# Performance work log

Hardware: AMD Instinct MI355X
Metric: run time of the kernel (lower is better)

The kernel has to match this reference:

```python
import jax, jax.numpy as jnp
import numpy as np

ATTN_SCALE = 0.12  # attn_args.attn_scale (constant hyperparameter)
EPS = 1e-6         # F.rms_norm eps
GATE_IN = 12       # attn_gate input features (x[..., :12])


def rms_norm(x):
    return x * jax.lax.rsqrt(jnp.mean(x * x, axis=-1, keepdims=True) + EPS)


def rotary(x, cos, sin):
    # x: [B,T,H,D]; cos/sin: [T,D//2]
    x1, x2 = jnp.split(x, 2, axis=-1)
    c = cos[None, :, None, :]
    s = sin[None, :, None, :]
    return jnp.concatenate([x1 * c + x2 * s, -x1 * s + x2 * c], axis=-1)


def setup_inputs() -> dict:
    key = jax.random.key(0)
    ks = jax.random.split(key, 5)
    B, T, D, H, HD = 1, 2048, 1024, 8, 128
    std = 0.5 * D ** -0.5
    x = jax.random.normal(ks[0], (B, T, D), jnp.float32)
    qkvo_w = jax.random.normal(ks[1], (4, D, D), jnp.float32) * std
    gate_w = jax.random.normal(ks[2], (H, GATE_IN), jnp.float32) * 0.02
    ve = jax.random.normal(ks[3], (B, T, H, HD), jnp.float32)
    sa_lambdas = jax.random.uniform(ks[4], (2,), jnp.float32, 0.3, 0.7)
    half = HD // 2
    inv_freq = 1.0 / (10000.0 ** (jnp.arange(half, dtype=jnp.float32) / half))
    ang = jnp.arange(T, dtype=jnp.float32)[:, None] * inv_freq[None, :]
    return dict(x=x, qkvo_w=qkvo_w, gate_w=gate_w, ve=ve,
                sa_lambdas=sa_lambdas, cos=jnp.cos(ang), sin=jnp.sin(ang))


def reference(x, qkvo_w, gate_w, ve, sa_lambdas, cos, sin):
    B, T, D = x.shape
    H = gate_w.shape[0]
    HD = D // H
    # fused QKV projection: rows of qkvo_w[:3] are [q; k; v]
    w_qkv = qkvo_w[:3].reshape(3 * D, D)           # [3D, D]
    qkv = jnp.einsum('btd,ed->bte', x, w_qkv)      # [B,T,3D]
    qkv = qkv.reshape(B, T, 3, H, HD)
    q, k, v = qkv[:, :, 0], qkv[:, :, 1], qkv[:, :, 2]
    # RMSNorm + RoPE on q, k
    q = rotary(rms_norm(q), cos, sin)
    k = rotary(rms_norm(k), cos, sin)
    # value-residual mixing
    v = sa_lambdas[0] * v + sa_lambdas[1] * ve
    # causal SDPA with custom scale
    scores = jnp.einsum('bqhd,bkhd->bhqk', q, k) * ATTN_SCALE
    causal = jnp.tril(jnp.ones((T, T), dtype=bool))
    scores = jnp.where(causal[None, None], scores, jnp.finfo(scores.dtype).min)
    p = jax.nn.softmax(scores, axis=-1)
    y = jnp.einsum('bhqk,bkhd->bqhd', p, v)        # [B,T,H,HD]
    # per-head sigmoid gate from the first 12 channels of x
    gate = jax.nn.sigmoid(jnp.einsum('bti,hi->bth', x[..., :GATE_IN], gate_w))
    y = y * gate[..., None]
    # output projection (qkvo_w[3]): F.linear -> y @ W_o^T
    out = jnp.einsum('bti,oi->bto', y.reshape(B, T, H * HD), qkvo_w[3])
    return out
```

## Files before the change

### kernel.cpp

```cpp
#include <hip/hip_runtime.h>
#include <stdint.h>

typedef unsigned short u16;
typedef unsigned int u32;

typedef __bf16 bfx8 __attribute__((ext_vector_type(8)));
typedef float fx4 __attribute__((ext_vector_type(4)));
typedef float fx16 __attribute__((ext_vector_type(16)));
typedef u16 u16x4 __attribute__((ext_vector_type(4)));
typedef u16 u16x8 __attribute__((ext_vector_type(8)));

#define GAS __attribute__((address_space(1)))
#define LAS __attribute__((address_space(3)))

__device__ __forceinline__ void gload16(const void* g, void* l) {
  __builtin_amdgcn_global_load_lds((GAS void*)g, (LAS void*)l, 16, 0, 0);
}

__device__ __forceinline__ u16 f2bf(float f) {
  union { float f; u32 u; } v; v.f = f;
  u32 r = v.u + 0x7fffu + ((v.u >> 16) & 1u);
  return (u16)(r >> 16);
}
__device__ __forceinline__ float bf2f(u16 u) {
  union { u32 u; float f; } v; v.u = ((u32)u) << 16;
  return v.f;
}

__device__ __forceinline__ int segF(int qb) { return (qb * qb + 2 * qb + (qb & 1)) >> 2; }

__global__ __launch_bounds__(256) void k_cvt(const float* __restrict__ src, u16* __restrict__ dst, int n) {
  int i = (blockIdx.x * 256 + threadIdx.x) * 8;
  if (i >= n) return;
  const float4* s = (const float4*)(src + i);
  float4 a = s[0], b = s[1];
  u16x8 o;
  o[0] = f2bf(a.x); o[1] = f2bf(a.y); o[2] = f2bf(a.z); o[3] = f2bf(a.w);
  o[4] = f2bf(b.x); o[5] = f2bf(b.y); o[6] = f2bf(b.z); o[7] = f2bf(b.w);
  *(u16x8*)(dst + i) = o;
}

__global__ __launch_bounds__(256) void k_gemm_out(const u16* __restrict__ A, const u16* __restrict__ B,
                                                  float* __restrict__ C, int M, int N, int K) {
  __shared__ char sm[16384];
  const int tid = threadIdx.x;
  const int l = tid & 63, w = tid >> 6;
  const int li = l & 15, lg = l >> 4;
  const int bid = (blockIdx.x & 7) * 64 + (blockIdx.x >> 3);
  const int nbm = M >> 6;
  const int bm = bid % nbm, bn = bid / nbm;

  const u16* gsrc[4];
#pragma unroll
  for (int i = 0; i < 4; ++i) {
    int b = i * 4096 + tid * 16;
    int row, ch;
    const u16* mat;
    if (b < 8192) { row = b >> 7; mat = A + (size_t)(bm * 64 + row) * K; }
    else          { int bb = b - 8192; row = bb >> 7; mat = B + (size_t)(bn * 64 + row) * K; }
    ch = ((b >> 4) & 7) ^ (row & 7);
    gsrc[i] = mat + ch * 8;
  }

  fx4 acc[4];
#pragma unroll
  for (int jj = 0; jj < 4; ++jj)
#pragma unroll
    for (int r = 0; r < 4; ++r) acc[jj][r] = 0.f;

  for (int k0 = 0; k0 < K; k0 += 64) {
    __syncthreads();
#pragma unroll
    for (int i = 0; i < 4; ++i) gload16(gsrc[i] + k0, sm + i * 4096 + w * 1024);
    __syncthreads();
#pragma unroll
    for (int kk = 0; kk < 2; ++kk) {
      int rowa = w * 16 + li;
      bfx8 af = *(const bfx8*)(sm + rowa * 128 + (((kk * 4 + lg)) ^ (rowa & 7)) * 16);
#pragma unroll
      for (int nf = 0; nf < 4; ++nf) {
        int rowb = nf * 16 + li;
        bfx8 bfr = *(const bfx8*)(sm + 8192 + rowb * 128 + ((kk * 4 + lg) ^ (rowb & 7)) * 16);
        acc[nf] = __builtin_amdgcn_mfma_f32_16x16x32_bf16(af, bfr, acc[nf], 0, 0, 0);
      }
    }
  }
#pragma unroll
  for (int nf = 0; nf < 4; ++nf)
#pragma unroll
    for (int r = 0; r < 4; ++r) {
      int row = bm * 64 + w * 16 + lg * 4 + r;
      int col = bn * 64 + nf * 16 + li;
      C[(size_t)row * N + col] = acc[nf][r];
    }
}

__global__ __launch_bounds__(256) void k_gemm_qkv(const u16* __restrict__ A, const u16* __restrict__ B,
                                                  u16* __restrict__ qb2, u16* __restrict__ kt2,
                                                  u16* __restrict__ vt2,
                                                  const float* __restrict__ ve, const float* __restrict__ lam,
                                                  const float* __restrict__ cosp, const float* __restrict__ sinp) {
  __shared__ char sm[24576];
  const int tid = threadIdx.x;
  const int l = tid & 63, w = tid >> 6;
  const int li = l & 15, lg = l >> 4;
  const int bid = (blockIdx.x & 7) * 96 + (blockIdx.x >> 3);
  const int bm = bid & 31, bn = bid >> 5;
  const int K = 1024;

  const u16* gsrc[6];
#pragma unroll
  for (int i = 0; i < 6; ++i) {
    int b = i * 4096 + tid * 16;
    int row, ch;
    const u16* mat;
    if (b < 8192) { row = b >> 7; mat = A + (size_t)(bm * 64 + row) * K; }
    else          { int bb = b - 8192; row = bb >> 7; mat = B + (size_t)(bn * 128 + row) * K; }
    ch = ((b >> 4) & 7) ^ (row & 7);
    gsrc[i] = mat + ch * 8;
  }

  fx4 acc[8];
#pragma unroll
  for (int jj = 0; jj < 8; ++jj)
#pragma unroll
    for (int r = 0; r < 4; ++r) acc[jj][r] = 0.f;

  for (int k0 = 0; k0 < K; k0 += 64) {
    __syncthreads();
#pragma unroll
    for (int i = 0; i < 6; ++i) gload16(gsrc[i] + k0, sm + i * 4096 + w * 1024);
    __syncthreads();
#pragma unroll
    for (int kk = 0; kk < 2; ++kk) {
      int rowa = w * 16 + li;
      bfx8 af = *(const bfx8*)(sm + rowa * 128 + ((kk * 4 + lg) ^ (rowa & 7)) * 16);
#pragma unroll
      for (int nf = 0; nf < 8; ++nf) {
        int rowb = nf * 16 + li;
        bfx8 bfr = *(const bfx8*)(sm + 8192 + rowb * 128 + ((kk * 4 + lg) ^ (rowb & 7)) * 16);
        acc[nf] = __builtin_amdgcn_mfma_f32_16x16x32_bf16(af, bfr, acc[nf], 0, 0, 0);
      }
    }
  }

  const int s = bn >> 3, h = bn & 7;
  if (s < 2) {
#pragma unroll
    for (int r = 0; r < 4; ++r) {
      int t = bm * 64 + w * 16 + lg * 4 + r;
      float ss = 0.f;
#pragma unroll
      for (int nf = 0; nf < 8; ++nf) ss += acc[nf][r] * acc[nf][r];
      ss += __shfl_xor(ss, 1); ss += __shfl_xor(ss, 2);
      ss += __shfl_xor(ss, 4); ss += __shfl_xor(ss, 8);
      float rn = rsqrtf(ss * (1.f / 128.f) + 1e-6f);
#pragma unroll
      for (int nf = 0; nf < 4; ++nf) {
        int dp = nf * 16 + li;
        float c = cosp[(size_t)t * 64 + dp];
        float sn = sinp[(size_t)t * 64 + dp];
        float x1 = acc[nf][r] * rn, x2 = acc[nf + 4][r] * rn;
        u16 o1 = f2bf(x1 * c + x2 * sn);
        u16 o2 = f2bf(-x1 * sn + x2 * c);
        if (s == 0) {
          u16* qp = qb2 + (size_t)t * 1024 + h * 128;
          qp[dp] = o1;
          qp[dp + 64] = o2;
        } else {
          u16* kp = kt2 + (size_t)h * 262144 + (size_t)(t >> 5) * 4096 + (t & 31) * 128;
          int dq = dp + 64;
          kp[(((dp >> 3) ^ (t & 7)) << 3) | (dp & 7)] = o1;
          kp[(((dq >> 3) ^ (t & 7)) << 3) | (dq & 7)] = o2;
        }
      }
    }
  } else {
    const float l0 = lam[0], l1 = lam[1];
    int tb = bm * 64 + w * 16 + lg * 4;
    u16* vbase = vt2 + (size_t)h * 262144 + (size_t)(tb >> 5) * 4096 + ((tb & 31) >> 3) * 1024 + (tb & 7);
#pragma unroll
    for (int nf = 0; nf < 8; ++nf) {
      int d = nf * 16 + li;
      u16x4 o;
#pragma unroll
      for (int r = 0; r < 4; ++r)
        o[r] = f2bf(l0 * acc[nf][r] + l1 * ve[(size_t)(tb + r) * 1024 + h * 128 + d]);
      *(u16x4*)(vbase + d * 8) = o;
    }
  }
}

__global__ __launch_bounds__(256) void k_attn2(const u16* __restrict__ qb2, const u16* __restrict__ kt2,
                                               const u16* __restrict__ vt2,
                                               u16* __restrict__ part, float* __restrict__ ml) {
  __shared__ char sm[32768];
  const int bid = (blockIdx.x & 7) * 72 + (blockIdx.x >> 3);
  const int h = bid / 72;
  const int r72 = bid % 72;
  int qb = 15;
  while (segF(qb) > r72) --qb;
  const int s = r72 - segF(qb);
  const int q0 = qb * 128;
  const int seg0 = s * 256;
  const int seg_len = min(256, (qb + 1) * 128 - seg0);
  const int nkt = seg_len >> 5;

  const int tid = threadIdx.x;
  const int l = tid & 63, w = tid >> 6;
  const int li = l & 31, hi = l >> 5;
  const int qrow = q0 + w * 32 + li;
  const int wqmax = q0 + w * 32 + 31;
  const int wqmin = q0 + w * 32;

  bfx8 Q[8];
  {
    const u16* qp = qb2 + (size_t)qrow * 1024 + h * 128 + hi * 8;
#pragma unroll
    for (int c = 0; c < 8; ++c) Q[c] = *(const bfx8*)(qp + c * 16);
  }

  const u16* ktile = kt2 + (size_t)h * 262144 + (size_t)(seg0 >> 5) * 4096;
  const u16* vtile = vt2 + (size_t)h * 262144 + (size_t)(seg0 >> 5) * 4096;

  auto STAGE = [&](int kt, int buf) {
    char* dst = sm + buf * 16384;
    const u16* ks = ktile + (size_t)kt * 4096;
    const u16* vs = vtile + (size_t)kt * 4096;
#pragma unroll
    for (int i = 0; i < 2; ++i) {
      int j = w * 2 + i;
      gload16(ks + j * 512 + l * 8, dst + j * 1024);
      gload16(vs + j * 512 + l * 8, dst + 8192 + j * 1024);
    }
  };

  fx16 Y[4];
#pragma unroll
  for (int d = 0; d < 4; ++d)
#pragma unroll
    for (int r = 0; r < 16; ++r) Y[d][r] = 0.f;
  float l_run = 0.f;

  STAGE(0, 0);
  __syncthreads();
  int cur = 0;

  for (int kt = 0; kt < nkt; ++kt) {
    if (kt + 1 < nkt) STAGE(kt + 1, cur ^ 1);
    const int k0 = seg0 + kt * 32;
    if (k0 <= wqmax) {
      const char* kb = sm + cur * 16384;
      const char* vb = kb + 8192;
      fx16 S;
#pragma unroll
      for (int r = 0; r < 16; ++r) S[r] = 0.f;
#pragma unroll
      for (int c = 0; c < 8; ++c) {
        int ch = (c * 2 + hi) ^ (li & 7);
        bfx8 kf = *(const bfx8*)(kb + li * 256 + ch * 16);
        S = __builtin_amdgcn_mfma_f32_32x32x16_bf16(kf, Q[c], S, 0, 0, 0);
      }
      const bool nomask = (k0 + 31 <= wqmin);
      float p[16];
      float ssum = 0.f;
      if (nomask) {
#pragma unroll
        for (int r = 0; r < 16; ++r) {
          float e = __expf(fmaf(S[r], 0.12f, -16.f));
          p[r] = e; ssum += e;
        }
      } else {
#pragma unroll
        for (int r = 0; r < 16; ++r) {
          int kk = (r & 3) + 8 * (r >> 2) + 4 * hi;
          float e = (k0 + kk <= qrow) ? __expf(fmaf(S[r], 0.12f, -16.f)) : 0.f;
          p[r] = e; ssum += e;
        }
      }
      ssum += __shfl_xor(ssum, 32);
      l_run += ssum;
      u32 pk[8], pks[8];
#pragma unroll
      for (int i = 0; i < 8; ++i) pk[i] = (u32)f2bf(p[2 * i]) | ((u32)f2bf(p[2 * i + 1]) << 16);
#pragma unroll
      for (int i = 0; i < 8; ++i) pks[i] = (u32)__shfl_xor((int)pk[i], 32);
      union { u32 u[4]; bfx8 v; } P0, P1;
      if (hi == 0) {
        P0.u[0] = pk[0];  P0.u[1] = pk[1];  P0.u[2] = pks[0]; P0.u[3] = pks[1];
        P1.u[0] = pk[4];  P1.u[1] = pk[5];  P1.u[2] = pks[4]; P1.u[3] = pks[5];
      } else {
        P0.u[0] = pks[2]; P0.u[1] = pks[3]; P0.u[2] = pk[2];  P0.u[3] = pk[3];
        P1.u[0] = pks[6]; P1.u[1] = pks[7]; P1.u[2] = pk[6];  P1.u[3] = pk[7];
      }
#pragma unroll
      for (int db = 0; db < 4; ++db) {
        int dd = db * 32 + li;
        bfx8 v0 = *(const bfx8*)(vb + hi * 2048 + dd * 16);
        bfx8 v1 = *(const bfx8*)(vb + (2 + hi) * 2048 + dd * 16);
        Y[db] = __builtin_amdgcn_mfma_f32_32x32x16_bf16(v0, P0.v, Y[db], 0, 0, 0);
        Y[db] = __builtin_amdgcn_mfma_f32_32x32x16_bf16(v1, P1.v, Y[db], 0, 0, 0);
      }
    }
    __syncthreads();
    cur ^= 1;
  }

  if (hi == 0) ml[(size_t)bid * 128 + w * 32 + li] = l_run;
  float* Yl = (float*)(sm + w * 8192);
  u16* pdst = part + (size_t)bid * 16384;
#pragma unroll
  for (int P = 0; P < 2; ++P) {
    asm volatile("" ::: "memory");
#pragma unroll
    for (int dh = 0; dh < 2; ++dh) {
      int db = P * 2 + dh;
#pragma unroll
      for (int r = 0; r < 16; ++r) {
        int dloc = dh * 32 + (r & 3) + 8 * (r >> 2) + 4 * hi;
        Yl[li * 64 + (dloc ^ ((li & 7) << 2))] = Y[db][r];
      }
    }
    asm volatile("" ::: "memory");
    int rr = l >> 1, c0 = (l & 1) * 32, sx = (rr & 7) << 2;
#pragma unroll
    for (int j = 0; j < 8; ++j) {
      float4 v = *(const float4*)(Yl + rr * 64 + ((c0 + j * 4) ^ sx));
      u16x4 o;
      o[0] = f2bf(v.x); o[1] = f2bf(v.y); o[2] = f2bf(v.z); o[3] = f2bf(v.w);
      *(u16x4*)(pdst + (w * 32 + rr) * 128 + P * 64 + c0 + j * 4) = o;
    }
  }
}

__global__ __launch_bounds__(256) void k_comb(const u16* __restrict__ part, const float* __restrict__ ml,
                                              const float* __restrict__ x, const float* __restrict__ gw,
                                              u16* __restrict__ y) {
  const int b = blockIdx.x;
  const int h = b >> 4, qb = b & 15;
  const int nseg = (qb + 2) >> 1;
  const int slot0 = h * 72 + segF(qb);
  const int t = threadIdx.x;
  const int r = t >> 1, hf = (t & 1) * 64;
  const int q = qb * 128 + r;

  float L = 0.f;
#pragma unroll
  for (int s = 0; s < 8; ++s)
    if (s < nseg) L += ml[(size_t)(slot0 + s) * 128 + r];

  float accv[64];
#pragma unroll
  for (int j = 0; j < 64; ++j) accv[j] = 0.f;
#pragma unroll
  for (int s = 0; s < 8; ++s) {
    if (s < nseg) {
      const u16x8* P = (const u16x8*)(part + (size_t)(slot0 + s) * 16384 + r * 128 + hf);
#pragma unroll
      for (int j = 0; j < 8; ++j) {
        u16x8 v = P[j];
#pragma unroll
        for (int e = 0; e < 8; ++e) accv[j * 8 + e] += bf2f(v[e]);
      }
    }
  }
  float dot = 0.f;
#pragma unroll
  for (int i = 0; i < 12; ++i) dot += x[(size_t)q * 1024 + i] * gw[h * 12 + i];
  float gt_ = 1.f / (1.f + __expf(-dot));
  float sc = gt_ / L;
  u16* yp = y + (size_t)q * 1024 + h * 128 + hf;
#pragma unroll
  for (int j = 0; j < 8; ++j) {
    u16x8 o;
#pragma unroll
    for (int e = 0; e < 8; ++e) o[e] = f2bf(accv[j * 8 + e] * sc);
    *(u16x8*)(yp + j * 8) = o;
  }
}

extern "C" void kernel_launch(void* const* d_in, const int* in_sizes, int n_in,
                              void* d_out, int out_size, void* d_ws, size_t ws_size,
                              hipStream_t stream) {
  const float* x = (const float*)d_in[0];
  const float* qkvo_w = (const float*)d_in[1];
  const float* gate_w = (const float*)d_in[2];
  const float* ve = (const float*)d_in[3];
  const float* lam = (const float*)d_in[4];
  const float* cosp = (const float*)d_in[5];
  const float* sinp = (const float*)d_in[6];
  float* out = (float*)d_out;

  u16* wb  = (u16*)d_ws;
  u16* xb  = wb + 4u * 1024 * 1024;
  u16* qb2 = xb + 2u * 1024 * 1024;
  u16* kt2 = qb2 + 2u * 1024 * 1024;
  u16* vt2 = kt2 + 2u * 1024 * 1024;
  u16* y   = vt2 + 2u * 1024 * 1024;
  u16* part = y + 2u * 1024 * 1024;
  float* ml = (float*)(part + (size_t)576 * 16384);

  k_cvt<<<dim3(2048), dim3(256), 0, stream>>>(qkvo_w, wb, 4 * 1024 * 1024);
  k_cvt<<<dim3(1024), dim3(256), 0, stream>>>(x, xb, 2 * 1024 * 1024);
  k_gemm_qkv<<<dim3(32 * 24), dim3(256), 0, stream>>>(xb, wb, qb2, kt2, vt2, ve, lam, cosp, sinp);
  k_attn2<<<dim3(576), dim3(256), 0, stream>>>(qb2, kt2, vt2, part, ml);
  k_comb<<<dim3(128), dim3(256), 0, stream>>>(part, ml, x, gate_w, y);
  k_gemm_out<<<dim3(32 * 16), dim3(256), 0, stream>>>(y, wb + 3u * 1024 * 1024, out, 2048, 1024, 1024);
}
```

Before: 97.75 us.

## Double-buffer GEMM LDS tiles and triple-buffer attention K/V prefetch

Both GEMM kernels get a second LDS buffer so the global-to-LDS load for the next K tile is issued before the MFMAs on the current tile run, with one barrier per iteration instead of two. The attention kernel moves from two K/V buffers to three, prefetching two tiles ahead and using an explicit vmcnt wait plus barrier, so each tile has more time to arrive. This doubles or raises shared memory per block, which may lower occupancy. The hand-written waitcnt also depends on the count of outstanding loads, so the tail iterations, where fewer loads are in flight, have to be handled correctly.

```diff
diff --git a/kernel.cpp b/kernel.cpp
--- a/kernel.cpp
+++ b/kernel.cpp
@@ -42,7 +42,7 @@
 
 __global__ __launch_bounds__(256) void k_gemm_out(const u16* __restrict__ A, const u16* __restrict__ B,
                                                   float* __restrict__ C, int M, int N, int K) {
-  __shared__ char sm[16384];
+  __shared__ char sm[32768];
   const int tid = threadIdx.x;
   const int l = tid & 63, w = tid >> 6;
   const int li = l & 15, lg = l >> 4;
@@ -68,22 +68,31 @@
 #pragma unroll
     for (int r = 0; r < 4; ++r) acc[jj][r] = 0.f;
 
+#pragma unroll
+  for (int i = 0; i < 4; ++i) gload16(gsrc[i], sm + i * 4096 + w * 1024);
+  __syncthreads();
+  int cur = 0;
+
   for (int k0 = 0; k0 < K; k0 += 64) {
-    __syncthreads();
-#pragma unroll
-    for (int i = 0; i < 4; ++i) gload16(gsrc[i] + k0, sm + i * 4096 + w * 1024);
-    __syncthreads();
+    if (k0 + 64 < K) {
+      char* dst = sm + (cur ^ 1) * 16384;
+#pragma unroll
+      for (int i = 0; i < 4; ++i) gload16(gsrc[i] + k0 + 64, dst + i * 4096 + w * 1024);
+    }
+    const char* base = sm + cur * 16384;
 #pragma unroll
     for (int kk = 0; kk < 2; ++kk) {
       int rowa = w * 16 + li;
-      bfx8 af = *(const bfx8*)(sm + rowa * 128 + (((kk * 4 + lg)) ^ (rowa & 7)) * 16);
+      bfx8 af = *(const bfx8*)(base + rowa * 128 + (((kk * 4 + lg)) ^ (rowa & 7)) * 16);
 #pragma unroll
       for (int nf = 0; nf < 4; ++nf) {
         int rowb = nf * 16 + li;
-        bfx8 bfr = *(const bfx8*)(sm + 8192 + rowb * 128 + ((kk * 4 + lg) ^ (rowb & 7)) * 16);
+        bfx8 bfr = *(const bfx8*)(base + 8192 + rowb * 128 + ((kk * 4 + lg) ^ (rowb & 7)) * 16);
         acc[nf] = __builtin_amdgcn_mfma_f32_16x16x32_bf16(af, bfr, acc[nf], 0, 0, 0);
       }
     }
+    __syncthreads();
+    cur ^= 1;
   }
 #pragma unroll
   for (int nf = 0; nf < 4; ++nf)
@@ -100,7 +109,7 @@
                                                   u16* __restrict__ vt2,
                                                   const float* __restrict__ ve, const float* __restrict__ lam,
                                                   const float* __restrict__ cosp, const float* __restrict__ sinp) {
-  __shared__ char sm[24576];
+  __shared__ char sm[49152];
   const int tid = threadIdx.x;
   const int l = tid & 63, w = tid >> 6;
   const int li = l & 15, lg = l >> 4;
@@ -126,22 +135,31 @@
 #pragma unroll
     for (int r = 0; r < 4; ++r) acc[jj][r] = 0.f;
 
+#pragma unroll
+  for (int i = 0; i < 6; ++i) gload16(gsrc[i], sm + i * 4096 + w * 1024);
+  __syncthreads();
+  int cur = 0;
+
   for (int k0 = 0; k0 < K; k0 += 64) {
-    __syncthreads();
-#pragma unroll
-    for (int i = 0; i < 6; ++i) gload16(gsrc[i] + k0, sm + i * 4096 + w * 1024);
-    __syncthreads();
+    if (k0 + 64 < K) {
+      char* dst = sm + (cur ^ 1) * 24576;
+#pragma unroll
+      for (int i = 0; i < 6; ++i) gload16(gsrc[i] + k0 + 64, dst + i * 4096 + w * 1024);
+    }
+    const char* base = sm + cur * 24576;
 #pragma unroll
     for (int kk = 0; kk < 2; ++kk) {
       int rowa = w * 16 + li;
-      bfx8 af = *(const bfx8*)(sm + rowa * 128 + ((kk * 4 + lg) ^ (rowa & 7)) * 16);
+      bfx8 af = *(const bfx8*)(base + rowa * 128 + ((kk * 4 + lg) ^ (rowa & 7)) * 16);
 #pragma unroll
       for (int nf = 0; nf < 8; ++nf) {
         int rowb = nf * 16 + li;
-        bfx8 bfr = *(const bfx8*)(sm + 8192 + rowb * 128 + ((kk * 4 + lg) ^ (rowb & 7)) * 16);
+        bfx8 bfr = *(const bfx8*)(base + 8192 + rowb * 128 + ((kk * 4 + lg) ^ (rowb & 7)) * 16);
         acc[nf] = __builtin_amdgcn_mfma_f32_16x16x32_bf16(af, bfr, acc[nf], 0, 0, 0);
       }
     }
+    __syncthreads();
+    cur ^= 1;
   }
 
   const int s = bn >> 3, h = bn & 7;
@@ -194,7 +212,7 @@
 __global__ __launch_bounds__(256) void k_attn2(const u16* __restrict__ qb2, const u16* __restrict__ kt2,
                                                const u16* __restrict__ vt2,
                                                u16* __restrict__ part, float* __restrict__ ml) {
-  __shared__ char sm[32768];
+  __shared__ char sm[49152];
   const int bid = (blockIdx.x & 7) * 72 + (blockIdx.x >> 3);
   const int h = bid / 72;
   const int r72 = bid % 72;
@@ -243,14 +261,14 @@
   float l_run = 0.f;
 
   STAGE(0, 0);
-  __syncthreads();
-  int cur = 0;
+  STAGE(1, 1);
 
   for (int kt = 0; kt < nkt; ++kt) {
-    if (kt + 1 < nkt) STAGE(kt + 1, cur ^ 1);
+    asm volatile("s_waitcnt vmcnt(4)\n\ts_barrier" ::: "memory");
+    if (kt + 2 < nkt) STAGE(kt + 2, (kt + 2) % 3);
     const int k0 = seg0 + kt * 32;
     if (k0 <= wqmax) {
-      const char* kb = sm + cur * 16384;
+      const char* kb = sm + (kt % 3) * 16384;
       const char* vb = kb + 8192;
       fx16 S;
 #pragma unroll
@@ -302,9 +320,8 @@
         Y[db] = __builtin_amdgcn_mfma_f32_32x32x16_bf16(v1, P1.v, Y[db], 0, 0, 0);
       }
     }
-    __syncthreads();
-    cur ^= 1;
-  }
+  }
+  __syncthreads();
 
   if (hi == 0) ml[(size_t)bid * 128 + w * 32 + li] = l_run;
   float* Yl = (float*)(sm + w * 8192);
```

Measured after the change: 95.38 us. 2.4% less time.
